# Kernel tuning notes

Measured on AMD Instinct MI355X. Metric: run time of the kernel, lower is better.

Reference implementation:

```python
import jax, jax.numpy as jnp
import numpy as np

EMBED_DIM = 1024
NUM_HEADS = 16
HEAD_DIM = EMBED_DIM // NUM_HEADS
B, T, S = 4, 2048, 2048


def setup_inputs() -> dict:
    key = jax.random.key(0)
    ks = jax.random.split(key, 11)
    sd = 1.0 / np.sqrt(EMBED_DIM)
    inp = {
        "query": jax.random.normal(ks[0], (B, T, EMBED_DIM), jnp.float32),
        "key": jax.random.normal(ks[1], (B, S, EMBED_DIM), jnp.float32),
        "value": jax.random.normal(ks[2], (B, S, EMBED_DIM), jnp.float32),
        # torch nn.Linear weights have shape (out_features, in_features)
        "Wq": jax.random.normal(ks[3], (EMBED_DIM, EMBED_DIM), jnp.float32) * sd,
        "bq": jnp.zeros((EMBED_DIM,), jnp.float32),
        "Wk": jax.random.normal(ks[4], (EMBED_DIM, EMBED_DIM), jnp.float32) * sd,
        "bk": jnp.zeros((EMBED_DIM,), jnp.float32),
        "Wv": jax.random.normal(ks[5], (EMBED_DIM, EMBED_DIM), jnp.float32) * sd,
        "bv": jnp.zeros((EMBED_DIM,), jnp.float32),
        "Wo": jax.random.normal(ks[6], (EMBED_DIM, EMBED_DIM), jnp.float32) * sd,
        "bo": jnp.zeros((EMBED_DIM,), jnp.float32),
    }
    return inp


def reference(query, key, value, Wq, bq, Wk, bk, Wv, bv, Wo, bo):
    scale = HEAD_DIM ** -0.5
    # projections (torch Linear: x @ W.T + b)
    q = query @ Wq.T + bq  # (B,T,C)
    k = key @ Wk.T + bk    # (B,S,C)
    v = value @ Wv.T + bv  # (B,S,C)
    # split heads -> (B,H,T,D)
    q = q.reshape(B, T, NUM_HEADS, HEAD_DIM).transpose(0, 2, 1, 3)
    k = k.reshape(B, S, NUM_HEADS, HEAD_DIM).transpose(0, 2, 1, 3)
    v = v.reshape(B, S, NUM_HEADS, HEAD_DIM).transpose(0, 2, 1, 3)
    # scores (B,H,T,S), softmax, weighted sum (dropout p=0 -> identity)
    scores = jnp.einsum("bhtd,bhsd->bhts", q, k) * scale
    attn = jax.nn.softmax(scores, axis=-1)
    out = jnp.einsum("bhts,bhsd->bhtd", attn, v)
    out = out.transpose(0, 2, 1, 3).reshape(B, T, EMBED_DIM)
    return out @ Wo.T + bo
```

## Files before the change

kernel.cpp:

```cpp
#include <hip/hip_runtime.h>
#include <math.h>
#include <stdint.h>

#define EMBED 1024
#define HEADS 16
#define HDIM  64
#define BATCH 4
#define SEQL  2048
#define MROWS (BATCH*SEQL)

typedef unsigned short u16;
typedef __bf16 bf16x8 __attribute__((ext_vector_type(8)));
typedef float  f32x16 __attribute__((ext_vector_type(16)));
typedef u16    u16x8  __attribute__((ext_vector_type(8)));

using gu32 = const __attribute__((address_space(1))) uint32_t;
using lu32 = __attribute__((address_space(3))) uint32_t;

#define LOG2E 1.44269504088896340736f

__device__ __forceinline__ u16 f2b(float f) {
  union { __bf16 h; u16 u; } c; c.h = (__bf16)f; return c.u;
}
__device__ __forceinline__ uint32_t pk2(float lo, float hi) {
  union { __bf16 h[2]; uint32_t u; } c;
  c.h[0] = (__bf16)lo; c.h[1] = (__bf16)hi;
  return c.u;
}

__global__ void cvt_bf16(const float* __restrict__ in, u16* __restrict__ out, int n4) {
  int i = blockIdx.x * blockDim.x + threadIdx.x;
  const int stride = gridDim.x * blockDim.x;
  for (; i < n4; i += stride) {
    float4 v = reinterpret_cast<const float4*>(in)[i];
    uint2 o; o.x = pk2(v.x, v.y); o.y = pk2(v.z, v.w);
    reinterpret_cast<uint2*>(out)[i] = o;
  }
}

template<int MODE>
__device__ __forceinline__ void gemm_core(const u16* __restrict__ A,
                                          const u16* __restrict__ W,
                                          const float* __restrict__ bias,
                                          void* __restrict__ outp, float scale,
                                          u16* As, u16* Bs)
{
  const int tid  = threadIdx.x;
  const int lane = tid & 63;
  const int wid  = tid >> 6;
  const int wm = wid >> 2, wn = wid & 3;
  const int l31 = lane & 31, hh = lane >> 5;
  const int bm = blockIdx.x * 128, bn = blockIdx.y * 128;

  f32x16 acc[2] = {};

  for (int k0 = 0; k0 < EMBED; k0 += 64) {
    __syncthreads();
#pragma unroll
    for (int r = 0; r < 2; ++r) {
      const int u = tid + r * 512;
      const int row = u >> 3, c = u & 7;
      __builtin_amdgcn_global_load_lds(
          (gu32*)(A + (size_t)(bm + row) * EMBED + k0 + c * 8),
          (lu32*)(As + (size_t)u * 8), 16, 0, 0);
      __builtin_amdgcn_global_load_lds(
          (gu32*)(W + (size_t)(bn + row) * EMBED + k0 + c * 8),
          (lu32*)(Bs + (size_t)u * 8), 16, 0, 0);
    }
    __syncthreads();

#pragma unroll
    for (int g = 0; g < 4; ++g) {
      bf16x8 af[2], bfr;
#pragma unroll
      for (int it = 0; it < 2; ++it) {
        const int row = wm * 64 + it * 32 + l31;
        af[it] = *reinterpret_cast<const bf16x8*>(As + row * 64 + g * 16 + hh * 8);
      }
      {
        const int row = wn * 32 + l31;
        bfr = *reinterpret_cast<const bf16x8*>(Bs + row * 64 + g * 16 + hh * 8);
      }
#pragma unroll
      for (int it = 0; it < 2; ++it)
        acc[it] = __builtin_amdgcn_mfma_f32_32x32x16_bf16(af[it], bfr, acc[it], 0, 0, 0);
    }
  }

  const int n = bn + wn * 32 + l31;
  const float bv = bias[n];
#pragma unroll
  for (int it = 0; it < 2; ++it) {
#pragma unroll
    for (int reg = 0; reg < 16; ++reg) {
      const int m = bm + wm * 64 + it * 32 + (reg & 3) + 8 * (reg >> 2) + 4 * hh;
      const float val = (acc[it][reg] + bv) * scale;
      if (MODE == 0) {
        ((float*)outp)[(size_t)m * EMBED + n] = val;
      } else {
        const int b = m >> 11, t = m & (SEQL - 1);
        const int h = n >> 6,  d = n & (HDIM - 1);
        ((u16*)outp)[(((size_t)(b * HEADS + h)) * SEQL + t) * HDIM + d] = f2b(val);
      }
    }
  }
}

__global__ __launch_bounds__(512)
void gemm_qkv(const u16* __restrict__ A0, const u16* __restrict__ A1, const u16* __restrict__ A2,
              const u16* __restrict__ W0, const u16* __restrict__ W1, const u16* __restrict__ W2,
              const float* __restrict__ b0, const float* __restrict__ b1, const float* __restrict__ b2,
              u16* __restrict__ o0, u16* __restrict__ o1, u16* __restrict__ o2,
              float s0)
{
  __shared__ __attribute__((aligned(16))) u16 As[128 * 64];
  __shared__ __attribute__((aligned(16))) u16 Bs[128 * 64];
  const int z = blockIdx.z;
  const u16*   A = (z == 0) ? A0 : (z == 1) ? A1 : A2;
  const u16*   W = (z == 0) ? W0 : (z == 1) ? W1 : W2;
  const float* b = (z == 0) ? b0 : (z == 1) ? b1 : b2;
  u16*         o = (z == 0) ? o0 : (z == 1) ? o1 : o2;
  const float  s = (z == 0) ? s0 : 1.f;
  gemm_core<1>(A, W, b, o, s, As, Bs);
}

__global__ __launch_bounds__(512)
void gemm_out(const u16* __restrict__ A, const u16* __restrict__ W,
              const float* __restrict__ bias, float* __restrict__ outp)
{
  __shared__ __attribute__((aligned(16))) u16 As[128 * 64];
  __shared__ __attribute__((aligned(16))) u16 Bs[128 * 64];
  gemm_core<0>(A, W, bias, outp, 1.f, As, Bs);
}

__global__ __launch_bounds__(256)
void attn_mfma(const u16* __restrict__ Qp, const u16* __restrict__ Kp,
               const u16* __restrict__ Vp, u16* __restrict__ Ob)
{
  __shared__ __attribute__((aligned(16))) u16 smem[128 * 66];
  u16* Ks = smem;
  u16* Vt = smem + 4096;

  const int tid  = threadIdx.x;
  const int lane = tid & 63;
  const int wq   = tid >> 6;
  const int l31  = lane & 31, hh = lane >> 5;
  const int bh   = blockIdx.y;
  const int q0   = blockIdx.x * 128;
  const size_t kvbase = (size_t)bh * SEQL * HDIM;

  bf16x8 qf[4];
  {
    const u16* qrow = Qp + kvbase + (size_t)(q0 + wq * 32 + l31) * HDIM;
#pragma unroll
    for (int g = 0; g < 4; ++g)
      qf[g] = *reinterpret_cast<const bf16x8*>(qrow + g * 16 + hh * 8);
  }

  float mrow = -INFINITY, lrow = 0.f;
  f32x16 oacc[2] = {};

  for (int s0 = 0; s0 < SEQL; s0 += 64) {
    __syncthreads();
#pragma unroll
    for (int r = 0; r < 2; ++r) {
      const int u = tid + r * 256;
      const int s = u >> 3, cc = u & 7;
      const int cg = cc ^ (s & 7);
      __builtin_amdgcn_global_load_lds(
          (gu32*)(Kp + kvbase + (size_t)(s0 + s) * HDIM + cg * 8),
          (lu32*)(Ks + (size_t)u * 8), 16, 0, 0);
    }
    u16x8 vreg[2];
#pragma unroll
    for (int r = 0; r < 2; ++r) {
      const int u = tid + r * 256;
      const int s = u >> 3, c = u & 7;
      vreg[r] = *reinterpret_cast<const u16x8*>(Vp + kvbase + (size_t)(s0 + s) * HDIM + c * 8);
    }
#pragma unroll
    for (int r = 0; r < 2; ++r) {
      const int u = tid + r * 256;
      const int s = u >> 3, c = u & 7;
#pragma unroll
      for (int e = 0; e < 8; ++e) {
        const int d = c * 8 + e;
        const int slot = (s >> 3) ^ (d & 7) ^ (d >> 3);
        Vt[d * 64 + slot * 8 + (s & 7)] = vreg[r][e];
      }
    }
    __syncthreads();

    f32x16 st[2] = {};
#pragma unroll
    for (int ts = 0; ts < 2; ++ts) {
      const int srow = ts * 32 + l31;
#pragma unroll
      for (int g = 0; g < 4; ++g) {
        const int slot = (g * 2 + hh) ^ (srow & 7);
        bf16x8 kf = *reinterpret_cast<const bf16x8*>(Ks + srow * 64 + slot * 8);
        st[ts] = __builtin_amdgcn_mfma_f32_32x32x16_bf16(kf, qf[g], st[ts], 0, 0, 0);
      }
    }

    float mx = -INFINITY;
#pragma unroll
    for (int ts = 0; ts < 2; ++ts)
#pragma unroll
      for (int rg = 0; rg < 16; ++rg) mx = fmaxf(mx, st[ts][rg]);
    mx = fmaxf(mx, __shfl_xor(mx, 32));
    if (!__all(mx <= mrow + 8.f)) {
      const float mnew = fmaxf(mrow, mx);
      const float alpha = __builtin_amdgcn_exp2f(mrow - mnew);
      lrow *= alpha;
#pragma unroll
      for (int jd = 0; jd < 2; ++jd)
#pragma unroll
        for (int rg = 0; rg < 16; ++rg) oacc[jd][rg] *= alpha;
      mrow = mnew;
    }
    float rsum = 0.f;
#pragma unroll
    for (int ts = 0; ts < 2; ++ts)
#pragma unroll
      for (int rg = 0; rg < 16; ++rg) {
        const float p = __builtin_amdgcn_exp2f(st[ts][rg] - mrow);
        st[ts][rg] = p;
        rsum += p;
      }
    rsum += __shfl_xor(rsum, 32);
    lrow += rsum;

    bf16x8 pb[4];
#pragma unroll
    for (int ts = 0; ts < 2; ++ts)
#pragma unroll
      for (int gl = 0; gl < 2; ++gl) {
        const int rb = gl * 8;
        const uint32_t A0 = pk2(st[ts][rb + 0], st[ts][rb + 1]);
        const uint32_t A1 = pk2(st[ts][rb + 2], st[ts][rb + 3]);
        const uint32_t B0 = pk2(st[ts][rb + 4], st[ts][rb + 5]);
        const uint32_t B1 = pk2(st[ts][rb + 6], st[ts][rb + 7]);
        const uint32_t sA0 = __shfl_xor(A0, 32);
        const uint32_t sA1 = __shfl_xor(A1, 32);
        const uint32_t sB0 = __shfl_xor(B0, 32);
        const uint32_t sB1 = __shfl_xor(B1, 32);
        union { uint32_t w[4]; bf16x8 v; } f;
        f.w[0] = hh ? sB0 : A0;
        f.w[1] = hh ? sB1 : A1;
        f.w[2] = hh ? B0  : sA0;
        f.w[3] = hh ? B1  : sA1;
        pb[ts * 2 + gl] = f.v;
      }

#pragma unroll
    for (int gs = 0; gs < 4; ++gs)
#pragma unroll
      for (int jd = 0; jd < 2; ++jd) {
        const int drow = jd * 32 + l31;
        const int slot = (gs * 2 + hh) ^ (drow & 7) ^ (drow >> 3);
        bf16x8 vf = *reinterpret_cast<const bf16x8*>(Vt + drow * 64 + slot * 8);
        oacc[jd] = __builtin_amdgcn_mfma_f32_32x32x16_bf16(vf, pb[gs], oacc[jd], 0, 0, 0);
      }
  }

  __syncthreads();
  u16* Os = smem;
  const float inv = 1.f / lrow;
  const int trow = wq * 32 + l31;
#pragma unroll
  for (int jd = 0; jd < 2; ++jd)
#pragma unroll
    for (int q = 0; q < 4; ++q) {
      const int dbase = jd * 32 + 8 * q + 4 * hh;
      const uint32_t w0 = pk2(oacc[jd][q * 4 + 0] * inv, oacc[jd][q * 4 + 1] * inv);
      const uint32_t w1 = pk2(oacc[jd][q * 4 + 2] * inv, oacc[jd][q * 4 + 3] * inv);
      *reinterpret_cast<uint32_t*>(Os + trow * 66 + dbase)     = w0;
      *reinterpret_cast<uint32_t*>(Os + trow * 66 + dbase + 2) = w1;
    }
  __syncthreads();
  const int b = bh >> 4, h = bh & 15;
#pragma unroll
  for (int r = 0; r < 4; ++r) {
    const int u = tid + r * 256;
    const int row = u >> 3, c = u & 7;
    uint32_t wds[4];
#pragma unroll
    for (int i2 = 0; i2 < 4; ++i2)
      wds[i2] = *reinterpret_cast<const uint32_t*>(Os + row * 66 + c * 8 + i2 * 2);
    uint4 ov; ov.x = wds[0]; ov.y = wds[1]; ov.z = wds[2]; ov.w = wds[3];
    *reinterpret_cast<uint4*>(Ob + ((size_t)(b * SEQL + q0 + row)) * EMBED + h * 64 + c * 8) = ov;
  }
}

extern "C" void kernel_launch(void* const* d_in, const int* in_sizes, int n_in,
                              void* d_out, int out_size, void* d_ws, size_t ws_size,
                              hipStream_t stream)
{
  const float* query = (const float*)d_in[0];
  const float* key   = (const float*)d_in[1];
  const float* value = (const float*)d_in[2];
  const float* Wq    = (const float*)d_in[3];
  const float* bq    = (const float*)d_in[4];
  const float* Wk    = (const float*)d_in[5];
  const float* bk    = (const float*)d_in[6];
  const float* Wv    = (const float*)d_in[7];
  const float* bv    = (const float*)d_in[8];
  const float* Wo    = (const float*)d_in[9];
  const float* bo    = (const float*)d_in[10];
  float* out = (float*)d_out;

  const size_t NBIG = (size_t)1 << 23;
  const size_t NW   = (size_t)1 << 20;
  u16* Xq  = (u16*)d_ws;
  u16* Xk  = Xq  + NBIG;
  u16* Xv  = Xk  + NBIG;
  u16* Wqb = Xv  + NBIG;
  u16* Wkb = Wqb + NW;
  u16* Wvb = Wkb + NW;
  u16* Wob = Wvb + NW;
  u16* Qb  = Wob + NW;
  u16* Kb  = Qb  + NBIG;
  u16* Vb  = Kb  + NBIG;
  u16* Oa  = Vb  + NBIG;

  cvt_bf16<<<2048, 256, 0, stream>>>(query, Xq, (int)(NBIG / 4));
  cvt_bf16<<<2048, 256, 0, stream>>>(key,   Xk, (int)(NBIG / 4));
  cvt_bf16<<<2048, 256, 0, stream>>>(value, Xv, (int)(NBIG / 4));
  cvt_bf16<<<512,  256, 0, stream>>>(Wq, Wqb, (int)(NW / 4));
  cvt_bf16<<<512,  256, 0, stream>>>(Wk, Wkb, (int)(NW / 4));
  cvt_bf16<<<512,  256, 0, stream>>>(Wv, Wvb, (int)(NW / 4));
  cvt_bf16<<<512,  256, 0, stream>>>(Wo, Wob, (int)(NW / 4));

  gemm_qkv<<<dim3(MROWS / 128, EMBED / 128, 3), 512, 0, stream>>>(
      Xq, Xk, Xv, Wqb, Wkb, Wvb, bq, bk, bv, Qb, Kb, Vb,
      0.125f * LOG2E);

  attn_mfma<<<dim3(SEQL / 128, BATCH * HEADS), 256, 0, stream>>>(Qb, Kb, Vb, Oa);

  gemm_out<<<dim3(MROWS / 128, EMBED / 128), 512, 0, stream>>>(Oa, Wob, bo, out);
}
```

Baseline: 496.1 us.

## Double-buffer K/V tiles in attention and enlarge per-wave GEMM tiles

The attention kernel now double-buffers K and V tiles in LDS, prefetching the next tile while computing on the current one, which leaves one barrier per iteration. It also raises MFMA priority with s_setprio, uses tree reductions for row max and sum, and sets launch bounds of 4 blocks per CU. The GEMMs move from 512 threads with 64x32 wave tiles to 256 threads with 64x64 wave tiles, giving more MFMA reuse per LDS fragment load. The costs are larger LDS use in attention (32KB) and more registers in the GEMM, which could lower occupancy.

After: 430.7 us. -13.2%, faster.

```diff
diff --git a/kernel.cpp b/kernel.cpp
--- a/kernel.cpp
+++ b/kernel.cpp
@@ -48,17 +48,17 @@
   const int tid  = threadIdx.x;
   const int lane = tid & 63;
   const int wid  = tid >> 6;
-  const int wm = wid >> 2, wn = wid & 3;
+  const int wm = wid >> 1, wn = wid & 1;
   const int l31 = lane & 31, hh = lane >> 5;
   const int bm = blockIdx.x * 128, bn = blockIdx.y * 128;
 
-  f32x16 acc[2] = {};
+  f32x16 acc[2][2] = {};
 
   for (int k0 = 0; k0 < EMBED; k0 += 64) {
     __syncthreads();
 #pragma unroll
-    for (int r = 0; r < 2; ++r) {
-      const int u = tid + r * 512;
+    for (int r = 0; r < 4; ++r) {
+      const int u = tid + r * 256;
       const int row = u >> 3, c = u & 7;
       __builtin_amdgcn_global_load_lds(
           (gu32*)(A + (size_t)(bm + row) * EMBED + k0 + c * 8),
@@ -71,42 +71,47 @@
 
 #pragma unroll
     for (int g = 0; g < 4; ++g) {
-      bf16x8 af[2], bfr;
+      bf16x8 af[2], bfr[2];
 #pragma unroll
       for (int it = 0; it < 2; ++it) {
         const int row = wm * 64 + it * 32 + l31;
         af[it] = *reinterpret_cast<const bf16x8*>(As + row * 64 + g * 16 + hh * 8);
       }
-      {
-        const int row = wn * 32 + l31;
-        bfr = *reinterpret_cast<const bf16x8*>(Bs + row * 64 + g * 16 + hh * 8);
+#pragma unroll
+      for (int jt = 0; jt < 2; ++jt) {
+        const int row = wn * 64 + jt * 32 + l31;
+        bfr[jt] = *reinterpret_cast<const bf16x8*>(Bs + row * 64 + g * 16 + hh * 8);
       }
 #pragma unroll
       for (int it = 0; it < 2; ++it)
-        acc[it] = __builtin_amdgcn_mfma_f32_32x32x16_bf16(af[it], bfr, acc[it], 0, 0, 0);
-    }
-  }
-
-  const int n = bn + wn * 32 + l31;
-  const float bv = bias[n];
-#pragma unroll
-  for (int it = 0; it < 2; ++it) {
-#pragma unroll
-    for (int reg = 0; reg < 16; ++reg) {
-      const int m = bm + wm * 64 + it * 32 + (reg & 3) + 8 * (reg >> 2) + 4 * hh;
-      const float val = (acc[it][reg] + bv) * scale;
-      if (MODE == 0) {
-        ((float*)outp)[(size_t)m * EMBED + n] = val;
-      } else {
-        const int b = m >> 11, t = m & (SEQL - 1);
-        const int h = n >> 6,  d = n & (HDIM - 1);
-        ((u16*)outp)[(((size_t)(b * HEADS + h)) * SEQL + t) * HDIM + d] = f2b(val);
-      }
-    }
-  }
-}
-
-__global__ __launch_bounds__(512)
+#pragma unroll
+        for (int jt = 0; jt < 2; ++jt)
+          acc[it][jt] = __builtin_amdgcn_mfma_f32_32x32x16_bf16(af[it], bfr[jt], acc[it][jt], 0, 0, 0);
+    }
+  }
+
+#pragma unroll
+  for (int it = 0; it < 2; ++it)
+#pragma unroll
+    for (int jt = 0; jt < 2; ++jt) {
+      const int n = bn + wn * 64 + jt * 32 + l31;
+      const float bv = bias[n];
+#pragma unroll
+      for (int reg = 0; reg < 16; ++reg) {
+        const int m = bm + wm * 64 + it * 32 + (reg & 3) + 8 * (reg >> 2) + 4 * hh;
+        const float val = (acc[it][jt][reg] + bv) * scale;
+        if (MODE == 0) {
+          ((float*)outp)[(size_t)m * EMBED + n] = val;
+        } else {
+          const int b = m >> 11, t = m & (SEQL - 1);
+          const int h = n >> 6,  d = n & (HDIM - 1);
+          ((u16*)outp)[(((size_t)(b * HEADS + h)) * SEQL + t) * HDIM + d] = f2b(val);
+        }
+      }
+    }
+}
+
+__global__ __launch_bounds__(256)
 void gemm_qkv(const u16* __restrict__ A0, const u16* __restrict__ A1, const u16* __restrict__ A2,
               const u16* __restrict__ W0, const u16* __restrict__ W1, const u16* __restrict__ W2,
               const float* __restrict__ b0, const float* __restrict__ b1, const float* __restrict__ b2,
@@ -124,7 +129,7 @@
   gemm_core<1>(A, W, b, o, s, As, Bs);
 }
 
-__global__ __launch_bounds__(512)
+__global__ __launch_bounds__(256)
 void gemm_out(const u16* __restrict__ A, const u16* __restrict__ W,
               const float* __restrict__ bias, float* __restrict__ outp)
 {
@@ -133,13 +138,11 @@
   gemm_core<0>(A, W, bias, outp, 1.f, As, Bs);
 }
 
-__global__ __launch_bounds__(256)
+__global__ __launch_bounds__(256, 4)
 void attn_mfma(const u16* __restrict__ Qp, const u16* __restrict__ Kp,
                const u16* __restrict__ Vp, u16* __restrict__ Ob)
 {
-  __shared__ __attribute__((aligned(16))) u16 smem[128 * 66];
-  u16* Ks = smem;
-  u16* Vt = smem + 4096;
+  __shared__ __attribute__((aligned(16))) u16 smem[16384];
 
   const int tid  = threadIdx.x;
   const int lane = tid & 63;
@@ -160,55 +163,81 @@
   float mrow = -INFINITY, lrow = 0.f;
   f32x16 oacc[2] = {};
 
-  for (int s0 = 0; s0 < SEQL; s0 += 64) {
-    __syncthreads();
+  {
 #pragma unroll
     for (int r = 0; r < 2; ++r) {
       const int u = tid + r * 256;
       const int s = u >> 3, cc = u & 7;
       const int cg = cc ^ (s & 7);
       __builtin_amdgcn_global_load_lds(
-          (gu32*)(Kp + kvbase + (size_t)(s0 + s) * HDIM + cg * 8),
-          (lu32*)(Ks + (size_t)u * 8), 16, 0, 0);
-    }
-    u16x8 vreg[2];
+          (gu32*)(Kp + kvbase + (size_t)s * HDIM + cg * 8),
+          (lu32*)(smem + (size_t)u * 8), 16, 0, 0);
+    }
 #pragma unroll
     for (int r = 0; r < 2; ++r) {
       const int u = tid + r * 256;
       const int s = u >> 3, c = u & 7;
-      vreg[r] = *reinterpret_cast<const u16x8*>(Vp + kvbase + (size_t)(s0 + s) * HDIM + c * 8);
-    }
-#pragma unroll
-    for (int r = 0; r < 2; ++r) {
-      const int u = tid + r * 256;
-      const int s = u >> 3, c = u & 7;
+      const u16x8 v = *reinterpret_cast<const u16x8*>(Vp + kvbase + (size_t)s * HDIM + c * 8);
 #pragma unroll
       for (int e = 0; e < 8; ++e) {
         const int d = c * 8 + e;
         const int slot = (s >> 3) ^ (d & 7) ^ (d >> 3);
-        Vt[d * 64 + slot * 8 + (s & 7)] = vreg[r][e];
-      }
-    }
-    __syncthreads();
+        smem[4096 + d * 64 + slot * 8 + (s & 7)] = v[e];
+      }
+    }
+  }
+  __syncthreads();
+
+  const int NT = SEQL / 64;
+  for (int t = 0; t < NT; ++t) {
+    const int cur = t & 1;
+    const u16* Kc = smem + cur * 8192;
+    const u16* Vc = smem + cur * 8192 + 4096;
+    u16* Kn = smem + (cur ^ 1) * 8192;
+    u16* Vn = smem + (cur ^ 1) * 8192 + 4096;
+    const bool pf = (t + 1 < NT);
+
+    u16x8 vreg[2];
+    if (pf) {
+      const int sb = (t + 1) * 64;
+#pragma unroll
+      for (int r = 0; r < 2; ++r) {
+        const int u = tid + r * 256;
+        const int s = u >> 3, cc = u & 7;
+        const int cg = cc ^ (s & 7);
+        __builtin_amdgcn_global_load_lds(
+            (gu32*)(Kp + kvbase + (size_t)(sb + s) * HDIM + cg * 8),
+            (lu32*)(Kn + (size_t)u * 8), 16, 0, 0);
+      }
+#pragma unroll
+      for (int r = 0; r < 2; ++r) {
+        const int u = tid + r * 256;
+        const int s = u >> 3, c = u & 7;
+        vreg[r] = *reinterpret_cast<const u16x8*>(Vp + kvbase + (size_t)(sb + s) * HDIM + c * 8);
+      }
+    }
 
     f32x16 st[2] = {};
-#pragma unroll
-    for (int ts = 0; ts < 2; ++ts) {
-      const int srow = ts * 32 + l31;
-#pragma unroll
-      for (int g = 0; g < 4; ++g) {
+    __builtin_amdgcn_s_setprio(1);
+#pragma unroll
+    for (int g = 0; g < 4; ++g)
+#pragma unroll
+      for (int ts = 0; ts < 2; ++ts) {
+        const int srow = ts * 32 + l31;
         const int slot = (g * 2 + hh) ^ (srow & 7);
-        bf16x8 kf = *reinterpret_cast<const bf16x8*>(Ks + srow * 64 + slot * 8);
+        bf16x8 kf = *reinterpret_cast<const bf16x8*>(Kc + srow * 64 + slot * 8);
         st[ts] = __builtin_amdgcn_mfma_f32_32x32x16_bf16(kf, qf[g], st[ts], 0, 0, 0);
       }
-    }
-
-    float mx = -INFINITY;
-#pragma unroll
-    for (int ts = 0; ts < 2; ++ts)
-#pragma unroll
-      for (int rg = 0; rg < 16; ++rg) mx = fmaxf(mx, st[ts][rg]);
-    mx = fmaxf(mx, __shfl_xor(mx, 32));
+    __builtin_amdgcn_s_setprio(0);
+
+    float red[16];
+#pragma unroll
+    for (int r = 0; r < 16; ++r) red[r] = fmaxf(st[0][r], st[1][r]);
+#pragma unroll
+    for (int off = 8; off >= 1; off >>= 1)
+#pragma unroll
+      for (int r = 0; r < off; ++r) red[r] = fmaxf(red[r], red[r + off]);
+    const float mx = fmaxf(red[0], __shfl_xor(red[0], 32));
     if (!__all(mx <= mrow + 8.f)) {
       const float mnew = fmaxf(mrow, mx);
       const float alpha = __builtin_amdgcn_exp2f(mrow - mnew);
@@ -219,17 +248,33 @@
         for (int rg = 0; rg < 16; ++rg) oacc[jd][rg] *= alpha;
       mrow = mnew;
     }
-    float rsum = 0.f;
 #pragma unroll
     for (int ts = 0; ts < 2; ++ts)
 #pragma unroll
-      for (int rg = 0; rg < 16; ++rg) {
-        const float p = __builtin_amdgcn_exp2f(st[ts][rg] - mrow);
-        st[ts][rg] = p;
-        rsum += p;
-      }
-    rsum += __shfl_xor(rsum, 32);
-    lrow += rsum;
+      for (int rg = 0; rg < 16; ++rg)
+        st[ts][rg] = __builtin_amdgcn_exp2f(st[ts][rg] - mrow);
+    float sr[16];
+#pragma unroll
+    for (int r = 0; r < 16; ++r) sr[r] = st[0][r] + st[1][r];
+#pragma unroll
+    for (int off = 8; off >= 1; off >>= 1)
+#pragma unroll
+      for (int r = 0; r < off; ++r) sr[r] += sr[r + off];
+    lrow += sr[0] + __shfl_xor(sr[0], 32);
+
+    if (pf) {
+#pragma unroll
+      for (int r = 0; r < 2; ++r) {
+        const int u = tid + r * 256;
+        const int s = u >> 3, c = u & 7;
+#pragma unroll
+        for (int e = 0; e < 8; ++e) {
+          const int d = c * 8 + e;
+          const int slot = (s >> 3) ^ (d & 7) ^ (d >> 3);
+          Vn[d * 64 + slot * 8 + (s & 7)] = vreg[r][e];
+        }
+      }
+    }
 
     bf16x8 pb[4];
 #pragma unroll
@@ -253,18 +298,21 @@
         pb[ts * 2 + gl] = f.v;
       }
 
+    __builtin_amdgcn_s_setprio(1);
 #pragma unroll
     for (int gs = 0; gs < 4; ++gs)
 #pragma unroll
       for (int jd = 0; jd < 2; ++jd) {
         const int drow = jd * 32 + l31;
         const int slot = (gs * 2 + hh) ^ (drow & 7) ^ (drow >> 3);
-        bf16x8 vf = *reinterpret_cast<const bf16x8*>(Vt + drow * 64 + slot * 8);
+        bf16x8 vf = *reinterpret_cast<const bf16x8*>(Vc + drow * 64 + slot * 8);
         oacc[jd] = __builtin_amdgcn_mfma_f32_32x32x16_bf16(vf, pb[gs], oacc[jd], 0, 0, 0);
       }
-  }
-
-  __syncthreads();
+    __builtin_amdgcn_s_setprio(0);
+
+    __syncthreads();
+  }
+
   u16* Os = smem;
   const float inv = 1.f / lrow;
   const int trow = wq * 32 + l31;
@@ -332,11 +380,11 @@
   cvt_bf16<<<512,  256, 0, stream>>>(Wv, Wvb, (int)(NW / 4));
   cvt_bf16<<<512,  256, 0, stream>>>(Wo, Wob, (int)(NW / 4));
 
-  gemm_qkv<<<dim3(MROWS / 128, EMBED / 128, 3), 512, 0, stream>>>(
+  gemm_qkv<<<dim3(MROWS / 128, EMBED / 128, 3), 256, 0, stream>>>(
       Xq, Xk, Xv, Wqb, Wkb, Wvb, bq, bk, bv, Qb, Kb, Vb,
       0.125f * LOG2E);
 
   attn_mfma<<<dim3(SEQL / 128, BATCH * HEADS), 256, 0, stream>>>(Qb, Kb, Vb, Oa);
 
-  gemm_out<<<dim3(MROWS / 128, EMBED / 128), 512, 0, stream>>>(Oa, Wob, bo, out);
-}
+  gemm_out<<<dim3(MROWS / 128, EMBED / 128), 256, 0, stream>>>(Oa, Wob, bo, out);
+}
```
